# Performance work log

Measured on AMD Instinct MI355X. Metric: run time of the kernel, lower is better.

Reference implementation:

```python
import jax, jax.numpy as jnp
import numpy as np


def setup_inputs() -> dict:
    key = jax.random.key(0)
    k1, k2 = jax.random.split(key)
    B, N1, N2, D = 4, 8192, 8192, 1
    x1 = jax.random.normal(k1, (B, N1, D), dtype=jnp.float32)
    x2 = jax.random.normal(k2, (B, N2, D), dtype=jnp.float32)
    scale = jnp.ones((D,), dtype=jnp.float32)  # nn.Parameter(torch.ones(input_dim))
    return {"x1": x1, "x2": x2, "scale": scale}


def reference(x1, x2, scale):
    # Pairwise squared distance: ||a||^2 + ||b||^2 - 2 a.b (avoids the
    # O(n1*n2*d) broadcast-diff intermediate of the torch code; same math).
    sq1 = jnp.sum(x1 * x1, axis=-1)  # [B, n1]
    sq2 = jnp.sum(x2 * x2, axis=-1)  # [B, n2]
    cross = jnp.einsum("bnd,bmd->bnm", x1, x2)  # [B, n1, n2]
    dist = sq1[:, :, None] + sq2[:, None, :] - 2.0 * cross
    # scale has shape [input_dim]=[1]; broadcasts over the kernel matrix.
    return jnp.exp(-dist / (2.0 * scale * scale))
```

## Files before the change

### kernel.cpp

```cpp
#include <hip/hip_runtime.h>
#include <hip/hip_bf16.h>


#define THREADS 256

typedef float vfloat4 __attribute__((ext_vector_type(4)));

__global__ __launch_bounds__(THREADS) void rbf_row_kernel(
    const float* __restrict__ x1,
    const float* __restrict__ x2,
    const float* __restrict__ scale,
    float* __restrict__ out,
    int N1, int N2) {
  const int row = blockIdx.x;
  const int b   = row / N1;
  const float a = x1[row];
  const float s = scale[0];
  const float c2 = -1.4426950408889634f / (2.0f * s * s);

  const vfloat4* __restrict__ x2v = (const vfloat4*)(x2 + (size_t)b * N2);
  vfloat4* __restrict__ outv = (vfloat4*)(out + (size_t)row * N2);

  const int n4 = N2 / 4;
  const int per_thread = n4 / THREADS;
  int j4 = threadIdx.x;
#pragma unroll
  for (int k = 0; k < 8; ++k) {
    if (k < per_thread || j4 < n4) {
      vfloat4 v = x2v[j4];
      vfloat4 d = a - v;
      vfloat4 r;
      r.x = exp2f(c2 * d.x * d.x);
      r.y = exp2f(c2 * d.y * d.y);
      r.z = exp2f(c2 * d.z * d.z);
      r.w = exp2f(c2 * d.w * d.w);
      __builtin_nontemporal_store(r, &outv[j4]);
    }
    j4 += THREADS;
  }
}

extern "C" void kernel_launch(void* const* d_in, const int* in_sizes, int n_in,
                              void* d_out, int out_size, void* d_ws, size_t ws_size,
                              hipStream_t stream) {
  const float* x1    = (const float*)d_in[0];
  const float* x2    = (const float*)d_in[1];
  const float* scale = (const float*)d_in[2];
  float* out = (float*)d_out;

  const int B  = 4;
  const int N1 = in_sizes[0] / B;
  const int N2 = in_sizes[1] / B;

  dim3 grid(B * N1);
  dim3 block(THREADS);
  rbf_row_kernel<<<grid, block, 0, stream>>>(x1, x2, scale, out, N1, N2);
}
```

Measured before the change: 1.030 ms.

## Process multiple rows per block and use hardware exp2 intrinsic

Each block now computes 8 output rows, reusing each loaded x2 vector across those rows, and the grid shrinks accordingly. exp2f is replaced by the raw amdgcn exp2 builtin to avoid extra range handling. The nontemporal store hint is dropped in favour of ordinary vector stores, which may change cache behaviour for this write-heavy output. A fallback with one row per block is kept when N1 is not divisible by 8.

```diff
diff --git a/kernel.cpp b/kernel.cpp
--- a/kernel.cpp
+++ b/kernel.cpp
@@ -1,42 +1,46 @@
 #include <hip/hip_runtime.h>
-#include <hip/hip_bf16.h>
 
 
 #define THREADS 256
+#define ROWS 8
 
 typedef float vfloat4 __attribute__((ext_vector_type(4)));
 
-__global__ __launch_bounds__(THREADS) void rbf_row_kernel(
+template <int R>
+__global__ __launch_bounds__(THREADS) void rbf_tile_kernel(
     const float* __restrict__ x1,
     const float* __restrict__ x2,
     const float* __restrict__ scale,
     float* __restrict__ out,
     int N1, int N2) {
-  const int row = blockIdx.x;
-  const int b   = row / N1;
-  const float a = x1[row];
-  const float s = scale[0];
+  const int row0 = blockIdx.x * R;
+  const int b    = row0 / N1;
+  const float s  = scale[0];
   const float c2 = -1.4426950408889634f / (2.0f * s * s);
 
+  float a[R];
+#pragma unroll
+  for (int r = 0; r < R; ++r) a[r] = x1[row0 + r];
+
   const vfloat4* __restrict__ x2v = (const vfloat4*)(x2 + (size_t)b * N2);
-  vfloat4* __restrict__ outv = (vfloat4*)(out + (size_t)row * N2);
+  float* const out0 = out + (size_t)row0 * N2;
+  const int n4 = N2 >> 2;
 
-  const int n4 = N2 / 4;
-  const int per_thread = n4 / THREADS;
-  int j4 = threadIdx.x;
+  for (int j4 = threadIdx.x; j4 < n4; j4 += THREADS) {
+    const vfloat4 v = x2v[j4];
 #pragma unroll
-  for (int k = 0; k < 8; ++k) {
-    if (k < per_thread || j4 < n4) {
-      vfloat4 v = x2v[j4];
-      vfloat4 d = a - v;
-      vfloat4 r;
-      r.x = exp2f(c2 * d.x * d.x);
-      r.y = exp2f(c2 * d.y * d.y);
-      r.z = exp2f(c2 * d.z * d.z);
-      r.w = exp2f(c2 * d.w * d.w);
-      __builtin_nontemporal_store(r, &outv[j4]);
+    for (int r = 0; r < R; ++r) {
+      vfloat4 d, e;
+      d.x = a[r] - v.x;
+      d.y = a[r] - v.y;
+      d.z = a[r] - v.z;
+      d.w = a[r] - v.w;
+      e.x = __builtin_amdgcn_exp2f(c2 * d.x * d.x);
+      e.y = __builtin_amdgcn_exp2f(c2 * d.y * d.y);
+      e.z = __builtin_amdgcn_exp2f(c2 * d.z * d.z);
+      e.w = __builtin_amdgcn_exp2f(c2 * d.w * d.w);
+      *(vfloat4*)(out0 + (size_t)r * N2 + ((size_t)j4 << 2)) = e;
     }
-    j4 += THREADS;
   }
 }
 
@@ -52,7 +56,11 @@
   const int N1 = in_sizes[0] / B;
   const int N2 = in_sizes[1] / B;
 
-  dim3 grid(B * N1);
-  dim3 block(THREADS);
-  rbf_row_kernel<<<grid, block, 0, stream>>>(x1, x2, scale, out, N1, N2);
+  if ((N1 % ROWS) == 0) {
+    dim3 grid((B * N1) / ROWS);
+    rbf_tile_kernel<ROWS><<<grid, dim3(THREADS), 0, stream>>>(x1, x2, scale, out, N1, N2);
+  } else {
+    dim3 grid(B * N1);
+    rbf_tile_kernel<1><<<grid, dim3(THREADS), 0, stream>>>(x1, x2, scale, out, N1, N2);
+  }
 }
```

Result: no change. 1.016 ms (-1.3%).

## Replace per-row blocks with grid-stride flat kernel and raw exp2 builtin

Applied to the files above, without the earlier changes.

Adds a persistent grid-stride kernel over the flattened output, using shift/mask indexing when sizes are powers of two, launched with a fixed 2048-block grid instead of one block per row. It uses the hardware exp2 builtin and drops the nontemporal store hint. The aim is to cut block scheduling overhead and index arithmetic. The trade-off is that regular stores may pollute the cache compared with nontemporal writes.

```diff
diff --git a/kernel.cpp b/kernel.cpp
--- a/kernel.cpp
+++ b/kernel.cpp
@@ -1,10 +1,45 @@
 #include <hip/hip_runtime.h>
-#include <hip/hip_bf16.h>
 
 
 #define THREADS 256
 
 typedef float vfloat4 __attribute__((ext_vector_type(4)));
+
+__global__ __launch_bounds__(THREADS) void rbf_flat_kernel(
+    const float* __restrict__ x1,
+    const float* __restrict__ x2,
+    const float* __restrict__ scale,
+    float* __restrict__ out,
+    int n4_total, int lg_n4row, int lg_N1) {
+  const float s  = scale[0];
+  const float c2 = -1.4426950408889634f / (2.0f * s * s);
+
+  const vfloat4* __restrict__ x2v = (const vfloat4*)x2;
+  vfloat4* __restrict__ outv = (vfloat4*)out;
+
+  const int j4mask = (1 << lg_n4row) - 1;
+  const int stride = gridDim.x * blockDim.x;
+
+#pragma unroll 4
+  for (int idx4 = blockIdx.x * blockDim.x + threadIdx.x; idx4 < n4_total;
+       idx4 += stride) {
+    const int row = idx4 >> lg_n4row;
+    const int j4  = idx4 & j4mask;
+    const int b   = row >> lg_N1;
+    const float a = x1[row];
+    const vfloat4 v = x2v[((size_t)b << lg_n4row) + j4];
+    vfloat4 d, e;
+    d.x = a - v.x;
+    d.y = a - v.y;
+    d.z = a - v.z;
+    d.w = a - v.w;
+    e.x = __builtin_amdgcn_exp2f(c2 * d.x * d.x);
+    e.y = __builtin_amdgcn_exp2f(c2 * d.y * d.y);
+    e.z = __builtin_amdgcn_exp2f(c2 * d.z * d.z);
+    e.w = __builtin_amdgcn_exp2f(c2 * d.w * d.w);
+    outv[idx4] = e;
+  }
+}
 
 __global__ __launch_bounds__(THREADS) void rbf_row_kernel(
     const float* __restrict__ x1,
@@ -17,28 +52,16 @@
   const float a = x1[row];
   const float s = scale[0];
   const float c2 = -1.4426950408889634f / (2.0f * s * s);
-
-  const vfloat4* __restrict__ x2v = (const vfloat4*)(x2 + (size_t)b * N2);
-  vfloat4* __restrict__ outv = (vfloat4*)(out + (size_t)row * N2);
-
-  const int n4 = N2 / 4;
-  const int per_thread = n4 / THREADS;
-  int j4 = threadIdx.x;
-#pragma unroll
-  for (int k = 0; k < 8; ++k) {
-    if (k < per_thread || j4 < n4) {
-      vfloat4 v = x2v[j4];
-      vfloat4 d = a - v;
-      vfloat4 r;
-      r.x = exp2f(c2 * d.x * d.x);
-      r.y = exp2f(c2 * d.y * d.y);
-      r.z = exp2f(c2 * d.z * d.z);
-      r.w = exp2f(c2 * d.w * d.w);
-      __builtin_nontemporal_store(r, &outv[j4]);
-    }
-    j4 += THREADS;
+  const float* x2r = x2 + (size_t)b * N2;
+  float* outr = out + (size_t)row * N2;
+  for (int j = threadIdx.x; j < N2; j += THREADS) {
+    const float d = a - x2r[j];
+    outr[j] = __builtin_amdgcn_exp2f(c2 * d * d);
   }
 }
+
+static inline bool is_pow2(int v) { return v > 0 && (v & (v - 1)) == 0; }
+static inline int ilog2(int v) { int l = 0; while ((1 << l) < v) ++l; return l; }
 
 extern "C" void kernel_launch(void* const* d_in, const int* in_sizes, int n_in,
                               void* d_out, int out_size, void* d_ws, size_t ws_size,
@@ -52,7 +75,14 @@
   const int N1 = in_sizes[0] / B;
   const int N2 = in_sizes[1] / B;
 
-  dim3 grid(B * N1);
-  dim3 block(THREADS);
-  rbf_row_kernel<<<grid, block, 0, stream>>>(x1, x2, scale, out, N1, N2);
+  if (is_pow2(N1) && is_pow2(N2) && (N2 % 4) == 0 && is_pow2(N2 / 4)) {
+    const int n4row = N2 / 4;
+    const int n4_total = B * N1 * n4row;
+    dim3 grid(2048);
+    rbf_flat_kernel<<<grid, dim3(THREADS), 0, stream>>>(
+        x1, x2, scale, out, n4_total, ilog2(n4row), ilog2(N1));
+  } else {
+    dim3 grid(B * N1);
+    rbf_row_kernel<<<grid, dim3(THREADS), 0, stream>>>(x1, x2, scale, out, N1, N2);
+  }
 }
```

After: 1.061 ms. 1.03x slower.
